# Optimization experiments

Measured on AMD Instinct MI355X. Metric: run time of the kernel, lower is better.

The kernel has to match this reference:

```python
import jax, jax.numpy as jnp
import numpy as np

BLOCK_SIZE = 128   # b
NUM_STEPS = 3      # T


def setup_inputs() -> dict:
    key = jax.random.key(0)
    kq, kk, kv = jax.random.split(key, 3)
    B, H, N, D = 4, 16, 8192, 64
    return {
        "query": jax.random.normal(kq, (B, H, N, D), jnp.float32),
        "key": jax.random.normal(kk, (B, H, N, D), jnp.float32),
        "value": jax.random.normal(kv, (B, H, N, D), jnp.float32),
    }


def reference(query, key, value):
    """Monarch attention: approximate softmax attention with a Monarch-factorized
    matrix M[(i,l),(k,l')] = L_l[i,k] * R_k[l,l'] (L: b blocks of m x m, R: m blocks
    of b x b, both row-stochastic), refined by NUM_STEPS alternating softmax updates.
    Never materializes the N x N attention matrix.
    """
    b, T = BLOCK_SIZE, NUM_STEPS
    B, H, N, D = query.shape
    m = N // b  # number of blocks; N assumed divisible by b (pad otherwise)
    scale = 1.0 / jnp.sqrt(jnp.asarray(D, query.dtype))
    eps = jnp.asarray(1e-6, query.dtype)

    Qb = query.reshape(B, H, m, b, D)   # token n = i*b + l -> (i, l)
    Kb = key.reshape(B, H, m, b, D)
    Vb = value.reshape(B, H, m, b, D)

    # init: uniform R  =>  Kbar[k,l] = mean_{l'} K[k,l'] (l-independent)
    Kbar = jnp.broadcast_to(Kb.mean(axis=3, keepdims=True), Qb.shape)  # (B,H,m,b,D)

    L = R = None
    for _ in range(T):
        # --- L update: L_l[i,k] = softmax_k( <Q[i,l], Kbar[k,l]> / sqrt(D) ) ---
        scores_L = scale * jnp.einsum('bhild,bhkld->bhlik', Qb, Kbar)  # (B,H,b,m,m)
        L = jax.nn.softmax(scores_L, axis=-1)
        # --- R update: weighted-average query per (k,l), then softmax over keys in block k ---
        w = jnp.sum(L, axis=-2)                                        # (B,H,b,m) = sum_i L_l[i,k]
        Qbar = jnp.einsum('bhlik,bhild->bhkld', L, Qb) / (jnp.swapaxes(w, -1, -2)[..., None] + eps)
        scores_R = scale * jnp.einsum('bhkld,bhked->bhkle', Qbar, Kb)  # (B,H,m,b,b) [k,l,l']
        R = jax.nn.softmax(scores_R, axis=-1)
        # refresh block-summarized keys for next L update
        Kbar = jnp.einsum('bhkle,bhked->bhkld', R, Kb)                 # (B,H,m,b,D)

    # output: out[(i,l)] = sum_k L_l[i,k] * (sum_{l'} R_k[l,l'] V[k,l'])
    Vbar = jnp.einsum('bhkle,bhked->bhkld', R, Vb)                     # (B,H,m,b,D)
    out = jnp.einsum('bhlik,bhkld->bhild', L, Vbar)                    # (B,H,m,b,D)
    return out.reshape(B, H, N, D)
```

## Files before the change

kernel.cpp:

```cpp
#include <hip/hip_runtime.h>
#include <stdint.h>


#define BH   64
#define NTOK 8192
#define DD   64
#define MM   64
#define BBS  128

typedef __attribute__((ext_vector_type(8))) short bf16x8;
typedef __attribute__((ext_vector_type(4))) float f32x4;

union U8 { bf16x8 v; uint32_t u[4]; };

__device__ __forceinline__ f32x4 MF(bf16x8 a, bf16x8 b, f32x4 c){
    return __builtin_amdgcn_mfma_f32_16x16x32_bf16(a, b, c, 0, 0, 0);
}
__device__ __forceinline__ f32x4 MF3(bf16x8 ah, bf16x8 al, bf16x8 bh_, bf16x8 bl_, f32x4 c){
    c = MF(ah, bh_, c);
    c = MF(ah, bl_, c);
    c = MF(al, bh_, c);
    return c;
}

__device__ __forceinline__ ushort bf16h(float x){
    union{float f; uint32_t u;} v; v.f = x;
    return (ushort)((v.u + 0x7fffu + ((v.u >> 16) & 1u)) >> 16);
}
__device__ __forceinline__ float bf16f(ushort h){
    union{float f; uint32_t u;} v; v.u = ((uint32_t)h) << 16; return v.f;
}
__device__ __forceinline__ void split2(float x, ushort& h, ushort& l){
    h = bf16h(x);
    l = bf16h(x - bf16f(h));
}
__device__ __forceinline__ uint32_t packsplit(float x){
    ushort h, l; split2(x, h, l);
    return ((uint32_t)h << 16) | (uint32_t)l;
}
__device__ __forceinline__ void st2(ushort* p, ushort a, ushort b){
    *(uint32_t*)p = (uint32_t)a | ((uint32_t)b << 16);
}
__device__ __forceinline__ void pack2(float a, float b, uint32_t& hw, uint32_t& lw){
    ushort ah_, al_, bh2, bl2;
    split2(a, ah_, al_); split2(b, bh2, bl2);
    hw = (uint32_t)ah_ | ((uint32_t)bh2 << 16);
    lw = (uint32_t)al_ | ((uint32_t)bl2 << 16);
}

__device__ __forceinline__ float red16_max(float v){
    v = fmaxf(v, __shfl_xor(v, 1));
    v = fmaxf(v, __shfl_xor(v, 2));
    v = fmaxf(v, __shfl_xor(v, 4));
    v = fmaxf(v, __shfl_xor(v, 8));
    return v;
}
__device__ __forceinline__ float red16_sum(float v){
    v += __shfl_xor(v, 1);
    v += __shfl_xor(v, 2);
    v += __shfl_xor(v, 4);
    v += __shfl_xor(v, 8);
    return v;
}

__device__ __forceinline__ void tr4x4(int qpos, float x0, float x1, float x2, float x3,
                                      float& z0, float& z1, float& z2, float& z3){
    float s1 = (qpos&1) ? x0 : x1; float g1 = __shfl_xor(s1, 16);
    float s2 = (qpos&1) ? x2 : x3; float g2 = __shfl_xor(s2, 16);
    float y0 = (qpos&1) ? g1 : x0;
    float y1 = (qpos&1) ? x1 : g1;
    float y2 = (qpos&1) ? g2 : x2;
    float y3 = (qpos&1) ? x3 : g2;
    float u1 = (qpos&2) ? y0 : y2; float h1 = __shfl_xor(u1, 32);
    float u2 = (qpos&2) ? y1 : y3; float h2 = __shfl_xor(u2, 32);
    z0 = (qpos&2) ? h1 : y0;
    z2 = (qpos&2) ? y2 : h1;
    z1 = (qpos&2) ? h2 : y1;
    z3 = (qpos&2) ? y3 : h2;
}

__global__ __launch_bounds__(256) void kbar0_kernel(const float* __restrict__ K,
                                                    float* __restrict__ kbar0){
    const int k = blockIdx.x, bh = blockIdx.y;
    const int t = threadIdx.x;
    const int d = t & 63, p = t >> 6;
    __shared__ float part[4][64];
    const float* base = K + ((size_t)bh*NTOK + (size_t)k*BBS)*DD + d;
    float s = 0.f;
    for(int lp = p*32; lp < p*32 + 32; ++lp) s += base[(size_t)lp*DD];
    part[p][d] = s;
    __syncthreads();
    if(t < 64){
        float tot = part[0][t] + part[1][t] + part[2][t] + part[3][t];
        kbar0[((size_t)bh*MM + k)*DD + t] = tot * (1.0f/128.0f);
    }
}

__global__ __launch_bounds__(256, 4) void l_kernel(const float* __restrict__ Q,
                                                   const void* __restrict__ kb_in,
                                                   int mode, uint32_t* __restrict__ qbar){
    const int l = blockIdx.x, bh = blockIdx.y;
    const int t = threadIdx.x;
    __shared__ __align__(16) ushort sQTh[64*72], sQTl[64*72];
    __shared__ __align__(16) ushort sKh [64*72], sKl [64*72];
    __shared__ float wsum[64];
    ushort* sLTh = sKh; ushort* sLTl = sKl;

    if(t < 64) wsum[t] = 0.f;

    const int w4 = t >> 4;
    const int qpos = w4 & 3;
    const int dq = (t & 15) << 2;
    #pragma unroll
    for(int j=0;j<4;++j){
        int i  = j*16 + w4;
        int ib = j*16 + (w4 & ~3);
        float4 v = *(const float4*)(Q + ((size_t)bh*NTOK + (size_t)i*BBS + l)*DD + dq);
        float z0,z1,z2,z3;
        tr4x4(qpos, v.x, v.y, v.z, v.w, z0, z1, z2, z3);
        ushort h0,l0,h1,l1,h2,l2,h3,l3;
        split2(z0,h0,l0); split2(z1,h1,l1); split2(z2,h2,l2); split2(z3,h3,l3);
        int rowd = dq + qpos;
        st2(&sQTh[rowd*72 + ib],   h0,h1); st2(&sQTh[rowd*72 + ib+2], h2,h3);
        st2(&sQTl[rowd*72 + ib],   l0,l1); st2(&sQTl[rowd*72 + ib+2], l2,l3);
    }
    if(mode){
        const uint32_t* kp = (const uint32_t*)kb_in + ((size_t)bh*BBS + l)*(size_t)(MM*DD);
        #pragma unroll
        for(int j=0;j<8;++j){
            int f = (j*256+t)*2, k = f>>6, d = f&63;
            uint2 u = *(const uint2*)(kp + (size_t)k*DD + d);
            *(uint32_t*)&sKh[k*72+d] = (u.x >> 16)      | (u.y & 0xffff0000u);
            *(uint32_t*)&sKl[k*72+d] = (u.x & 0xffffu)  | (u.y << 16);
        }
    } else {
        const float* kp = (const float*)kb_in + (size_t)bh*(size_t)(MM*DD);
        #pragma unroll
        for(int j=0;j<4;++j){
            int idx = j*256+t, k = idx>>4, d = (idx&15)<<2;
            float4 v = *(const float4*)(kp + (size_t)k*DD + d);
            ushort h0,l0,h1,l1,h2,l2,h3,l3;
            split2(v.x,h0,l0); split2(v.y,h1,l1); split2(v.z,h2,l2); split2(v.w,h3,l3);
            st2(&sKh[k*72+d],   h0,h1); st2(&sKh[k*72+d+2], h2,h3);
            st2(&sKl[k*72+d],   l0,l1); st2(&sKl[k*72+d+2], l2,l3);
        }
    }
    __syncthreads();

    const int lane = t & 63, wv = t >> 6;
    const int n = lane & 15, qd = lane >> 4;
    const int m0 = wv * 16;

    f32x4 accS[4] = {};
    #pragma unroll
    for(int kb=0;kb<2;++kb){
        int co = kb*32 + qd*8;
        U8 ah, al;
        #pragma unroll
        for(int jj=0;jj<4;++jj){
            uint32_t a0 = sQTh[(co+2*jj  )*72 + m0+n];
            uint32_t a1 = sQTh[(co+2*jj+1)*72 + m0+n];
            ah.u[jj] = a0 | (a1<<16);
            uint32_t b0 = sQTl[(co+2*jj  )*72 + m0+n];
            uint32_t b1 = sQTl[(co+2*jj+1)*72 + m0+n];
            al.u[jj] = b0 | (b1<<16);
        }
        #pragma unroll
        for(int c=0;c<4;++c){
            bf16x8 bh_ = *(const bf16x8*)&sKh[(c*16+n)*72 + co];
            bf16x8 bl_ = *(const bf16x8*)&sKl[(c*16+n)*72 + co];
            accS[c] = MF3(ah.v, al.v, bh_, bl_, accS[c]);
        }
    }
    __syncthreads();

    float colp[4] = {0.f,0.f,0.f,0.f};
    #pragma unroll
    for(int r=0;r<4;++r){
        float vals[4]; float mx = -3.4e38f;
        #pragma unroll
        for(int c=0;c<4;++c){ vals[c] = accS[c][r]*0.125f; mx = fmaxf(mx, vals[c]); }
        mx = red16_max(mx);
        float s = 0.f;
        #pragma unroll
        for(int c=0;c<4;++c){ vals[c] = __expf(vals[c]-mx); s += vals[c]; }
        s = red16_sum(s);
        float inv = 1.0f/s;
        int irow = m0 + qd*4 + r;
        #pragma unroll
        for(int c=0;c<4;++c){
            float Lv = vals[c]*inv;
            colp[c] += Lv;
            ushort hh, ll; split2(Lv, hh, ll);
            sLTh[(c*16+n)*72 + irow] = hh;
            sLTl[(c*16+n)*72 + irow] = ll;
        }
    }
    #pragma unroll
    for(int c=0;c<4;++c){
        float v = colp[c];
        v += __shfl_xor(v,16); v += __shfl_xor(v,32);
        if(qd == 0) atomicAdd(&wsum[c*16+n], v);
    }
    __syncthreads();

    f32x4 accQ[4] = {};
    #pragma unroll
    for(int kb=0;kb<2;++kb){
        int co = kb*32 + qd*8;
        bf16x8 ah = *(const bf16x8*)&sLTh[(m0+n)*72 + co];
        bf16x8 al = *(const bf16x8*)&sLTl[(m0+n)*72 + co];
        #pragma unroll
        for(int dt2=0;dt2<4;++dt2){
            bf16x8 bh_ = *(const bf16x8*)&sQTh[(dt2*16+n)*72 + co];
            bf16x8 bl_ = *(const bf16x8*)&sQTl[(dt2*16+n)*72 + co];
            accQ[dt2] = MF3(ah, al, bh_, bl_, accQ[dt2]);
        }
    }
    uint32_t* qb = qbar + ((size_t)bh*BBS + l)*(size_t)(MM*DD);
    #pragma unroll
    for(int r=0;r<4;++r){
        int krow = m0 + qd*4 + r;
        float invw = 1.0f/(wsum[krow] + 1e-6f);
        #pragma unroll
        for(int dt2=0;dt2<4;++dt2){
            qb[(size_t)krow*DD + dt2*16 + n] = packsplit(accQ[dt2][r]*invw);
        }
    }
}

__global__ __launch_bounds__(512, 4) void r_kernel(const uint32_t* __restrict__ qbar,
                                                   const float* __restrict__ K,
                                                   const float* __restrict__ V,
                                                   uint32_t* __restrict__ outp, int outTok){
    const int k = blockIdx.x, bh = blockIdx.y;
    const int t = threadIdx.x;
    __shared__ __align__(16) ushort sm[32768];
    ushort* X1h = sm;
    ushort* X1l = sm + 8192;
    ushort* XTh = sm + 16384;
    ushort* XTl = sm + 24576;

    const int lane = t & 63, wv = t >> 6;
    const int n = lane & 15, qd = lane >> 4;
    const int m0 = wv * 16;

    const uint32_t* qrow = qbar + (size_t)bh*BBS*(size_t)(MM*DD) + (size_t)k*DD
                         + (size_t)(m0+n)*(size_t)(MM*DD);
    uint4 qa0 = *(const uint4*)(qrow + qd*8);
    uint4 qa1 = *(const uint4*)(qrow + qd*8 + 4);
    uint4 qa2 = *(const uint4*)(qrow + 32 + qd*8);
    uint4 qa3 = *(const uint4*)(qrow + 32 + qd*8 + 4);

    const float* kp = K + ((size_t)bh*NTOK + (size_t)k*BBS)*DD;
    const float* vp = V ? (V + ((size_t)bh*NTOK + (size_t)k*BBS)*DD) : kp;
    const int w4 = t >> 4;
    const int qpos = w4 & 3;
    const int dq = (t & 15) << 2;
    #pragma unroll
    for(int j=0;j<4;++j){
        int lp = j*32 + w4;
        float4 v = *(const float4*)(kp + (size_t)lp*DD + dq);
        ushort h0,l0,h1,l1,h2,l2,h3,l3;
        split2(v.x,h0,l0); split2(v.y,h1,l1); split2(v.z,h2,l2); split2(v.w,h3,l3);
        int e = ((lp>>2)<<8) + (((dq>>4)&3)<<6) + ((lp&3)<<4) + ((dq&15) ^ (((dq>>4)&1)<<3));
        st2(&X1h[e], h0,h1); st2(&X1h[e+2], h2,h3);
        st2(&X1l[e], l0,l1); st2(&X1l[e+2], l2,l3);

        float4 tv = v;
        if(V) tv = *(const float4*)(vp + (size_t)lp*DD + dq);
        float z0,z1,z2,z3;
        tr4x4(qpos, tv.x, tv.y, tv.z, tv.w, z0, z1, z2, z3);
        int dv = dq + qpos;
        int lb = j*32 + (w4 & ~3);
        ushort th0,tl0,th1,tl1,th2,tl2,th3,tl3;
        split2(z0,th0,tl0); split2(z1,th1,tl1); split2(z2,th2,tl2); split2(z3,th3,tl3);
        int eT = ((dv>>2)<<9) + ((lb>>4)<<6) + ((dv&3)<<4) + ((lb&15) ^ (((dv>>2)&1)<<3));
        st2(&XTh[eT], th0,th1); st2(&XTh[eT+2], th2,th3);
        st2(&XTl[eT], tl0,tl1); st2(&XTl[eT+2], tl2,tl3);
    }
    __syncthreads();

    U8 ah0, al0, ah1, al1;
    ah0.u[0] = (qa0.x>>16) | (qa0.y & 0xffff0000u);
    al0.u[0] = (qa0.x & 0xffffu) | (qa0.y<<16);
    ah0.u[1] = (qa0.z>>16) | (qa0.w & 0xffff0000u);
    al0.u[1] = (qa0.z & 0xffffu) | (qa0.w<<16);
    ah0.u[2] = (qa1.x>>16) | (qa1.y & 0xffff0000u);
    al0.u[2] = (qa1.x & 0xffffu) | (qa1.y<<16);
    ah0.u[3] = (qa1.z>>16) | (qa1.w & 0xffff0000u);
    al0.u[3] = (qa1.z & 0xffffu) | (qa1.w<<16);
    ah1.u[0] = (qa2.x>>16) | (qa2.y & 0xffff0000u);
    al1.u[0] = (qa2.x & 0xffffu) | (qa2.y<<16);
    ah1.u[1] = (qa2.z>>16) | (qa2.w & 0xffff0000u);
    al1.u[1] = (qa2.z & 0xffffu) | (qa2.w<<16);
    ah1.u[2] = (qa3.x>>16) | (qa3.y & 0xffff0000u);
    al1.u[2] = (qa3.x & 0xffffu) | (qa3.y<<16);
    ah1.u[3] = (qa3.z>>16) | (qa3.w & 0xffff0000u);
    al1.u[3] = (qa3.z & 0xffffu) | (qa3.w<<16);

    const int base1 = (n>>2)*256 + (n&3)*16 + ((qd>>1)<<6) + ((8*(qd&1)) ^ (8*((qd>>1)&1)));
    f32x4 accS[8] = {};
    #pragma unroll
    for(int c=0;c<8;++c){
        bf16x8 bh_ = *(const bf16x8*)&X1h[base1 + c*1024];
        bf16x8 bl_ = *(const bf16x8*)&X1l[base1 + c*1024];
        accS[c] = MF3(ah0.v, al0.v, bh_, bl_, accS[c]);
    }
    #pragma unroll
    for(int c=0;c<8;++c){
        bf16x8 bh_ = *(const bf16x8*)&X1h[base1 + c*1024 + 128];
        bf16x8 bl_ = *(const bf16x8*)&X1l[base1 + c*1024 + 128];
        accS[c] = MF3(ah1.v, al1.v, bh_, bl_, accS[c]);
    }

    #pragma unroll
    for(int r=0;r<4;++r){
        float vals[8]; float mx = -3.4e38f;
        #pragma unroll
        for(int c=0;c<8;++c){ vals[c] = accS[c][r]*0.125f; mx = fmaxf(mx, vals[c]); }
        mx = red16_max(mx);
        float s = 0.f;
        #pragma unroll
        for(int c=0;c<8;++c){ vals[c] = __expf(vals[c]-mx); s += vals[c]; }
        s = red16_sum(s);
        float inv = 1.0f/s;
        #pragma unroll
        for(int c=0;c<8;++c) accS[c][r] = vals[c]*inv;
    }
    __syncthreads();

    ushort* SWh = sm + wv*1280;
    ushort* SWl = SWh + 640;
    const int sw_rd = n*40 + qd*8;
    const int baseT = (n>>2)*512 + ((qd>>1)<<6) + (n&3)*16 + ((8*(qd&1)) ^ (8*((n>>2)&1)));
    f32x4 accO[4] = {};
    #pragma unroll
    for(int kb=0;kb<4;++kb){
        #pragma unroll
        for(int r=0;r<4;++r){
            #pragma unroll
            for(int c2=0;c2<2;++c2){
                ushort hh, ll;
                split2(accS[2*kb+c2][r], hh, ll);
                SWh[(qd*4+r)*40 + c2*16 + n] = hh;
                SWl[(qd*4+r)*40 + c2*16 + n] = ll;
            }
        }
        asm volatile("s_waitcnt lgkmcnt(0)" ::: "memory");
        __builtin_amdgcn_sched_barrier(0);
        bf16x8 ah2 = *(const bf16x8*)&SWh[sw_rd];
        bf16x8 al2 = *(const bf16x8*)&SWl[sw_rd];
        #pragma unroll
        for(int dt2=0;dt2<4;++dt2){
            bf16x8 bh_ = *(const bf16x8*)&XTh[baseT + dt2*2048 + kb*128];
            bf16x8 bl_ = *(const bf16x8*)&XTl[baseT + dt2*2048 + kb*128];
            accO[dt2] = MF3(ah2, al2, bh_, bl_, accO[dt2]);
        }
        asm volatile("" ::: "memory");
    }
    #pragma unroll
    for(int r=0;r<4;++r){
        int lrow = m0 + qd*4 + r;
        #pragma unroll
        for(int dt2=0;dt2<4;++dt2){
            uint32_t pw = packsplit(accO[dt2][r]);
            size_t off = outTok
                ? ((size_t)bh*NTOK + (size_t)k*BBS + lrow)*DD + dt2*16 + n
                : (((size_t)bh*BBS + lrow)*(size_t)MM + k)*DD + dt2*16 + n;
            outp[off] = pw;
        }
    }
}

__global__ __launch_bounds__(256, 4) void out_kernel(const float* __restrict__ Q,
                                                     const uint32_t* __restrict__ kbar,
                                                     float* __restrict__ out){
    const int l = blockIdx.x, bh = blockIdx.y;
    const int t = threadIdx.x;
    __shared__ __align__(16) ushort sKh [64*72], sKl [64*72];
    __shared__ __align__(16) ushort sVTh[64*72], sVTl[64*72];
    ushort* sLh = sKh; ushort* sLl = sKl;

    const int lane = t & 63, wv = t >> 6;
    const int n = lane & 15, qd = lane >> 4;
    const int m0 = wv * 16;

    const float* qr = Q + ((size_t)bh*NTOK + (size_t)(m0+n)*BBS + l)*DD;
    float4 qv0 = *(const float4*)(qr + qd*8);
    float4 qv1 = *(const float4*)(qr + qd*8 + 4);
    float4 qv2 = *(const float4*)(qr + 32 + qd*8);
    float4 qv3 = *(const float4*)(qr + 32 + qd*8 + 4);

    const uint32_t* kp = kbar + ((size_t)bh*BBS + l)*(size_t)(MM*DD);
    #pragma unroll
    for(int j=0;j<8;++j){
        int f = (j*256+t)*2, k = f>>6, d = f&63;
        uint2 u = *(const uint2*)(kp + (size_t)k*DD + d);
        *(uint32_t*)&sKh[k*72+d] = (u.x >> 16)     | (u.y & 0xffff0000u);
        *(uint32_t*)&sKl[k*72+d] = (u.x & 0xffffu) | (u.y << 16);
    }
    const uint32_t* vb = (const uint32_t*)out;
    #pragma unroll
    for(int j=0;j<16;++j){
        int idx = j*256+t, kk = idx>>6, d = idx&63;
        uint32_t u = vb[((size_t)bh*NTOK + (size_t)kk*BBS + l)*DD + d];
        sVTh[d*72+kk] = (ushort)(u >> 16);
        sVTl[d*72+kk] = (ushort)(u & 0xffffu);
    }
    __syncthreads();

    U8 ah0, al0, ah1, al1;
    pack2(qv0.x, qv0.y, ah0.u[0], al0.u[0]);
    pack2(qv0.z, qv0.w, ah0.u[1], al0.u[1]);
    pack2(qv1.x, qv1.y, ah0.u[2], al0.u[2]);
    pack2(qv1.z, qv1.w, ah0.u[3], al0.u[3]);
    pack2(qv2.x, qv2.y, ah1.u[0], al1.u[0]);
    pack2(qv2.z, qv2.w, ah1.u[1], al1.u[1]);
    pack2(qv3.x, qv3.y, ah1.u[2], al1.u[2]);
    pack2(qv3.z, qv3.w, ah1.u[3], al1.u[3]);

    f32x4 accS[4] = {};
    #pragma unroll
    for(int kb=0;kb<2;++kb){
        int co = kb*32 + qd*8;
        const bf16x8 ah = kb ? ah1.v : ah0.v;
        const bf16x8 al = kb ? al1.v : al0.v;
        #pragma unroll
        for(int c=0;c<4;++c){
            bf16x8 bh_ = *(const bf16x8*)&sKh[(c*16+n)*72 + co];
            bf16x8 bl_ = *(const bf16x8*)&sKl[(c*16+n)*72 + co];
            accS[c] = MF3(ah, al, bh_, bl_, accS[c]);
        }
    }
    __syncthreads();

    #pragma unroll
    for(int r=0;r<4;++r){
        float vals[4]; float mx = -3.4e38f;
        #pragma unroll
        for(int c=0;c<4;++c){ vals[c] = accS[c][r]*0.125f; mx = fmaxf(mx, vals[c]); }
        mx = red16_max(mx);
        float s = 0.f;
        #pragma unroll
        for(int c=0;c<4;++c){ vals[c] = __expf(vals[c]-mx); s += vals[c]; }
        s = red16_sum(s);
        float inv = 1.0f/s;
        int irow = m0 + qd*4 + r;
        #pragma unroll
        for(int c=0;c<4;++c){
            ushort hh, ll; split2(vals[c]*inv, hh, ll);
            sLh[irow*72 + c*16+n] = hh;
            sLl[irow*72 + c*16+n] = ll;
        }
    }
    __syncthreads();

    f32x4 accO[4] = {};
    #pragma unroll
    for(int kb=0;kb<2;++kb){
        int co = kb*32 + qd*8;
        bf16x8 ah = *(const bf16x8*)&sLh[(m0+n)*72 + co];
        bf16x8 al = *(const bf16x8*)&sLl[(m0+n)*72 + co];
        #pragma unroll
        for(int dt2=0;dt2<4;++dt2){
            bf16x8 bh_ = *(const bf16x8*)&sVTh[(dt2*16+n)*72 + co];
            bf16x8 bl_ = *(const bf16x8*)&sVTl[(dt2*16+n)*72 + co];
            accO[dt2] = MF3(ah, al, bh_, bl_, accO[dt2]);
        }
    }
    #pragma unroll
    for(int r=0;r<4;++r){
        int irow = m0 + qd*4 + r;
        #pragma unroll
        for(int dt2=0;dt2<4;++dt2){
            out[((size_t)bh*NTOK + (size_t)irow*BBS + l)*DD + dt2*16 + n] = accO[dt2][r];
        }
    }
}

extern "C" void kernel_launch(void* const* d_in, const int* in_sizes, int n_in,
                              void* d_out, int out_size, void* d_ws, size_t ws_size,
                              hipStream_t stream){
    const float* Q = (const float*)d_in[0];
    const float* K = (const float*)d_in[1];
    const float* V = (const float*)d_in[2];
    float* out = (float*)d_out;
    const size_t big = (size_t)BH * BBS * MM * DD;
    uint32_t* qbar  = (uint32_t*)d_ws;
    uint32_t* kbar  = qbar + big;
    float*    kbar0 = (float*)(kbar + big);

    kbar0_kernel<<<dim3(MM, BH), 256, 0, stream>>>(K, kbar0);
    l_kernel<<<dim3(BBS, BH), 256, 0, stream>>>(Q, kbar0, 0, qbar);
    r_kernel<<<dim3(MM, BH), 512, 0, stream>>>(qbar, K, nullptr, kbar, 0);
    l_kernel<<<dim3(BBS, BH), 256, 0, stream>>>(Q, kbar, 1, qbar);
    r_kernel<<<dim3(MM, BH), 512, 0, stream>>>(qbar, K, nullptr, kbar, 0);
    l_kernel<<<dim3(BBS, BH), 256, 0, stream>>>(Q, kbar, 1, qbar);
    r_kernel<<<dim3(MM, BH), 512, 0, stream>>>(qbar, K, V, (uint32_t*)out, 1);
    out_kernel<<<dim3(BBS, BH), 256, 0, stream>>>(Q, kbar, out);
}
```

Before: 1.022 ms.

## Cache pre-split bf16 Q/K in workspace, load Kbar fragments directly, swizzle LDS

```diff
diff --git a/kernel.cpp b/kernel.cpp
--- a/kernel.cpp
+++ b/kernel.cpp
@@ -41,11 +41,24 @@
 __device__ __forceinline__ void st2(ushort* p, ushort a, ushort b){
     *(uint32_t*)p = (uint32_t)a | ((uint32_t)b << 16);
 }
+__device__ __forceinline__ void up2(uint32_t w0, uint32_t w1, uint32_t& hw, uint32_t& lw){
+    hw = (w0 >> 16)     | (w1 & 0xffff0000u);
+    lw = (w0 & 0xffffu) | (w1 << 16);
+}
 __device__ __forceinline__ void pack2(float a, float b, uint32_t& hw, uint32_t& lw){
     ushort ah_, al_, bh2, bl2;
     split2(a, ah_, al_); split2(b, bh2, bl2);
     hw = (uint32_t)ah_ | ((uint32_t)bh2 << 16);
     lw = (uint32_t)al_ | ((uint32_t)bl2 << 16);
+}
+__device__ __forceinline__ int swz8(int row){
+    return ((((row & 3) << 1) ^ ((row >> 2) & 7)) << 3);
+}
+__device__ __forceinline__ void frag_pk(uint4 a, uint4 b, bf16x8& h, bf16x8& l){
+    U8 H, L;
+    up2(a.x,a.y,H.u[0],L.u[0]); up2(a.z,a.w,H.u[1],L.u[1]);
+    up2(b.x,b.y,H.u[2],L.u[2]); up2(b.z,b.w,H.u[3],L.u[3]);
+    h = H.v; l = L.v;
 }
 
 __device__ __forceinline__ float red16_max(float v){
@@ -63,16 +76,16 @@
     return v;
 }
 
-__device__ __forceinline__ void tr4x4(int qpos, float x0, float x1, float x2, float x3,
-                                      float& z0, float& z1, float& z2, float& z3){
-    float s1 = (qpos&1) ? x0 : x1; float g1 = __shfl_xor(s1, 16);
-    float s2 = (qpos&1) ? x2 : x3; float g2 = __shfl_xor(s2, 16);
-    float y0 = (qpos&1) ? g1 : x0;
-    float y1 = (qpos&1) ? x1 : g1;
-    float y2 = (qpos&1) ? g2 : x2;
-    float y3 = (qpos&1) ? x3 : g2;
-    float u1 = (qpos&2) ? y0 : y2; float h1 = __shfl_xor(u1, 32);
-    float u2 = (qpos&2) ? y1 : y3; float h2 = __shfl_xor(u2, 32);
+__device__ __forceinline__ void tr4x4u(int qpos, uint32_t x0, uint32_t x1, uint32_t x2, uint32_t x3,
+                                       uint32_t& z0, uint32_t& z1, uint32_t& z2, uint32_t& z3){
+    uint32_t s1 = (qpos&1) ? x0 : x1; uint32_t g1 = (uint32_t)__shfl_xor((int)s1, 16);
+    uint32_t s2 = (qpos&1) ? x2 : x3; uint32_t g2 = (uint32_t)__shfl_xor((int)s2, 16);
+    uint32_t y0 = (qpos&1) ? g1 : x0;
+    uint32_t y1 = (qpos&1) ? x1 : g1;
+    uint32_t y2 = (qpos&1) ? g2 : x2;
+    uint32_t y3 = (qpos&1) ? x3 : g2;
+    uint32_t u1 = (qpos&2) ? y0 : y2; uint32_t h1 = (uint32_t)__shfl_xor((int)u1, 32);
+    uint32_t u2 = (qpos&2) ? y1 : y3; uint32_t h2 = (uint32_t)__shfl_xor((int)u2, 32);
     z0 = (qpos&2) ? h1 : y0;
     z2 = (qpos&2) ? y2 : h1;
     z1 = (qpos&2) ? h2 : y1;
@@ -80,99 +93,113 @@
 }
 
 __global__ __launch_bounds__(256) void kbar0_kernel(const float* __restrict__ K,
-                                                    float* __restrict__ kbar0){
+                                                    uint32_t* __restrict__ kbar0p,
+                                                    uint32_t* __restrict__ kpk){
     const int k = blockIdx.x, bh = blockIdx.y;
     const int t = threadIdx.x;
     const int d = t & 63, p = t >> 6;
     __shared__ float part[4][64];
     const float* base = K + ((size_t)bh*NTOK + (size_t)k*BBS)*DD + d;
+    uint32_t* kpb = kpk ? kpk + ((size_t)bh*NTOK + (size_t)k*BBS)*DD + d : nullptr;
     float s = 0.f;
-    for(int lp = p*32; lp < p*32 + 32; ++lp) s += base[(size_t)lp*DD];
+    for(int lp = p*32; lp < p*32 + 32; ++lp){
+        float v = base[(size_t)lp*DD];
+        s += v;
+        if(kpb) kpb[(size_t)lp*DD] = packsplit(v);
+    }
     part[p][d] = s;
     __syncthreads();
     if(t < 64){
         float tot = part[0][t] + part[1][t] + part[2][t] + part[3][t];
-        kbar0[((size_t)bh*MM + k)*DD + t] = tot * (1.0f/128.0f);
+        kbar0p[((size_t)bh*MM + k)*DD + t] = packsplit(tot * (1.0f/128.0f));
     }
 }
 
 __global__ __launch_bounds__(256, 4) void l_kernel(const float* __restrict__ Q,
-                                                   const void* __restrict__ kb_in,
-                                                   int mode, uint32_t* __restrict__ qbar){
+                                                   const uint32_t* __restrict__ kb_in,
+                                                   int mode,
+                                                   const uint32_t* __restrict__ qpk_ld,
+                                                   uint32_t* __restrict__ qpk_st,
+                                                   uint32_t* __restrict__ qbar){
     const int l = blockIdx.x, bh = blockIdx.y;
     const int t = threadIdx.x;
-    __shared__ __align__(16) ushort sQTh[64*72], sQTl[64*72];
-    __shared__ __align__(16) ushort sKh [64*72], sKl [64*72];
+    __shared__ __align__(16) ushort sQTh[4096], sQTl[4096];
+    __shared__ __align__(16) ushort sLTh[4096], sLTl[4096];
     __shared__ float wsum[64];
-    ushort* sLTh = sKh; ushort* sLTl = sKl;
+
+    const int lane = t & 63, wv = t >> 6;
+    const int n = lane & 15, qd = lane >> 4;
+    const int m0 = wv * 16;
 
     if(t < 64) wsum[t] = 0.f;
 
-    const int w4 = t >> 4;
-    const int qpos = w4 & 3;
-    const int dq = (t & 15) << 2;
+    U8 ah0, al0, ah1, al1;
+    const size_t qoff = ((size_t)bh*NTOK + (size_t)(m0+n)*BBS + l)*DD;
+    if(qpk_ld){
+        uint4 a0 = *(const uint4*)(qpk_ld + qoff + qd*8);
+        uint4 a1 = *(const uint4*)(qpk_ld + qoff + qd*8 + 4);
+        uint4 a2 = *(const uint4*)(qpk_ld + qoff + 32 + qd*8);
+        uint4 a3 = *(const uint4*)(qpk_ld + qoff + 32 + qd*8 + 4);
+        up2(a0.x,a0.y,ah0.u[0],al0.u[0]); up2(a0.z,a0.w,ah0.u[1],al0.u[1]);
+        up2(a1.x,a1.y,ah0.u[2],al0.u[2]); up2(a1.z,a1.w,ah0.u[3],al0.u[3]);
+        up2(a2.x,a2.y,ah1.u[0],al1.u[0]); up2(a2.z,a2.w,ah1.u[1],al1.u[1]);
+        up2(a3.x,a3.y,ah1.u[2],al1.u[2]); up2(a3.z,a3.w,ah1.u[3],al1.u[3]);
+    } else {
+        float4 qv0 = *(const float4*)(Q + qoff + qd*8);
+        float4 qv1 = *(const float4*)(Q + qoff + qd*8 + 4);
+        float4 qv2 = *(const float4*)(Q + qoff + 32 + qd*8);
+        float4 qv3 = *(const float4*)(Q + qoff + 32 + qd*8 + 4);
+        pack2(qv0.x,qv0.y,ah0.u[0],al0.u[0]); pack2(qv0.z,qv0.w,ah0.u[1],al0.u[1]);
+        pack2(qv1.x,qv1.y,ah0.u[2],al0.u[2]); pack2(qv1.z,qv1.w,ah0.u[3],al0.u[3]);
+        pack2(qv2.x,qv2.y,ah1.u[0],al1.u[0]); pack2(qv2.z,qv2.w,ah1.u[1],al1.u[1]);
+        pack2(qv3.x,qv3.y,ah1.u[2],al1.u[2]); pack2(qv3.z,qv3.w,ah1.u[3],al1.u[3]);
+    }
+
+    const int w4 = t >> 4, qpos = w4 & 3, dq = (t & 15) << 2;
     #pragma unroll
     for(int j=0;j<4;++j){
         int i  = j*16 + w4;
         int ib = j*16 + (w4 & ~3);
-        float4 v = *(const float4*)(Q + ((size_t)bh*NTOK + (size_t)i*BBS + l)*DD + dq);
-        float z0,z1,z2,z3;
-        tr4x4(qpos, v.x, v.y, v.z, v.w, z0, z1, z2, z3);
-        ushort h0,l0,h1,l1,h2,l2,h3,l3;
-        split2(z0,h0,l0); split2(z1,h1,l1); split2(z2,h2,l2); split2(z3,h3,l3);
+        size_t off = ((size_t)bh*NTOK + (size_t)i*BBS + l)*DD + dq;
+        uint32_t p0,p1,p2,p3v;
+        if(qpk_ld){
+            uint4 u = *(const uint4*)(qpk_ld + off);
+            p0=u.x; p1=u.y; p2=u.z; p3v=u.w;
+        } else {
+            float4 v = *(const float4*)(Q + off);
+            p0=packsplit(v.x); p1=packsplit(v.y); p2=packsplit(v.z); p3v=packsplit(v.w);
+            if(qpk_st){
+                uint4 uu; uu.x=p0; uu.y=p1; uu.z=p2; uu.w=p3v;
+                *(uint4*)(qpk_st + off) = uu;
+            }
+        }
+        uint32_t z0,z1,z2,z3;
+        tr4x4u(qpos, p0,p1,p2,p3v, z0,z1,z2,z3);
         int rowd = dq + qpos;
-        st2(&sQTh[rowd*72 + ib],   h0,h1); st2(&sQTh[rowd*72 + ib+2], h2,h3);
-        st2(&sQTl[rowd*72 + ib],   l0,l1); st2(&sQTl[rowd*72 + ib+2], l2,l3);
-    }
-    if(mode){
-        const uint32_t* kp = (const uint32_t*)kb_in + ((size_t)bh*BBS + l)*(size_t)(MM*DD);
-        #pragma unroll
-        for(int j=0;j<8;++j){
-            int f = (j*256+t)*2, k = f>>6, d = f&63;
-            uint2 u = *(const uint2*)(kp + (size_t)k*DD + d);
-            *(uint32_t*)&sKh[k*72+d] = (u.x >> 16)      | (u.y & 0xffff0000u);
-            *(uint32_t*)&sKl[k*72+d] = (u.x & 0xffffu)  | (u.y << 16);
-        }
-    } else {
-        const float* kp = (const float*)kb_in + (size_t)bh*(size_t)(MM*DD);
-        #pragma unroll
-        for(int j=0;j<4;++j){
-            int idx = j*256+t, k = idx>>4, d = (idx&15)<<2;
-            float4 v = *(const float4*)(kp + (size_t)k*DD + d);
-            ushort h0,l0,h1,l1,h2,l2,h3,l3;
-            split2(v.x,h0,l0); split2(v.y,h1,l1); split2(v.z,h2,l2); split2(v.w,h3,l3);
-            st2(&sKh[k*72+d],   h0,h1); st2(&sKh[k*72+d+2], h2,h3);
-            st2(&sKl[k*72+d],   l0,l1); st2(&sKl[k*72+d+2], l2,l3);
-        }
-    }
-    __syncthreads();
-
-    const int lane = t & 63, wv = t >> 6;
-    const int n = lane & 15, qd = lane >> 4;
-    const int m0 = wv * 16;
-
+        int e = rowd*64 + (ib ^ swz8(rowd));
+        st2(&sQTh[e],   (ushort)(z0>>16), (ushort)(z1>>16));
+        st2(&sQTh[e+2], (ushort)(z2>>16), (ushort)(z3>>16));
+        st2(&sQTl[e],   (ushort)(z0&0xffffu), (ushort)(z1&0xffffu));
+        st2(&sQTl[e+2], (ushort)(z2&0xffffu), (ushort)(z3&0xffffu));
+    }
+    __syncthreads();
+
+    const uint32_t* kb_base = mode ? kb_in + ((size_t)bh*BBS + l)*(size_t)(MM*DD)
+                                   : kb_in + (size_t)bh*(size_t)(MM*DD);
     f32x4 accS[4] = {};
     #pragma unroll
     for(int kb=0;kb<2;++kb){
-        int co = kb*32 + qd*8;
-        U8 ah, al;
-        #pragma unroll
-        for(int jj=0;jj<4;++jj){
-            uint32_t a0 = sQTh[(co+2*jj  )*72 + m0+n];
-            uint32_t a1 = sQTh[(co+2*jj+1)*72 + m0+n];
-            ah.u[jj] = a0 | (a1<<16);
-            uint32_t b0 = sQTl[(co+2*jj  )*72 + m0+n];
-            uint32_t b1 = sQTl[(co+2*jj+1)*72 + m0+n];
-            al.u[jj] = b0 | (b1<<16);
-        }
+        bf16x8 ah = kb ? ah1.v : ah0.v;
+        bf16x8 al = kb ? al1.v : al0.v;
         #pragma unroll
         for(int c=0;c<4;++c){
-            bf16x8 bh_ = *(const bf16x8*)&sKh[(c*16+n)*72 + co];
-            bf16x8 bl_ = *(const bf16x8*)&sKl[(c*16+n)*72 + co];
-            accS[c] = MF3(ah.v, al.v, bh_, bl_, accS[c]);
-        }
-    }
-    __syncthreads();
+            const uint32_t* fp = kb_base + (size_t)(c*16+n)*DD + kb*32 + qd*8;
+            uint4 b0 = *(const uint4*)fp;
+            uint4 b1 = *(const uint4*)(fp + 4);
+            bf16x8 bh_, bl_; frag_pk(b0, b1, bh_, bl_);
+            accS[c] = MF3(ah, al, bh_, bl_, accS[c]);
+        }
+    }
 
     float colp[4] = {0.f,0.f,0.f,0.f};
     #pragma unroll
@@ -192,8 +219,9 @@
             float Lv = vals[c]*inv;
             colp[c] += Lv;
             ushort hh, ll; split2(Lv, hh, ll);
-            sLTh[(c*16+n)*72 + irow] = hh;
-            sLTl[(c*16+n)*72 + irow] = ll;
+            int row = c*16+n;
+            sLTh[row*64 + (irow ^ swz8(row))] = hh;
+            sLTl[row*64 + (irow ^ swz8(row))] = ll;
         }
     }
     #pragma unroll
@@ -208,12 +236,14 @@
     #pragma unroll
     for(int kb=0;kb<2;++kb){
         int co = kb*32 + qd*8;
-        bf16x8 ah = *(const bf16x8*)&sLTh[(m0+n)*72 + co];
-        bf16x8 al = *(const bf16x8*)&sLTl[(m0+n)*72 + co];
+        int ra = m0 + n;
+        bf16x8 ah = *(const bf16x8*)&sLTh[ra*64 + (co ^ swz8(ra))];
+        bf16x8 al = *(const bf16x8*)&sLTl[ra*64 + (co ^ swz8(ra))];
         #pragma unroll
         for(int dt2=0;dt2<4;++dt2){
-            bf16x8 bh_ = *(const bf16x8*)&sQTh[(dt2*16+n)*72 + co];
-            bf16x8 bl_ = *(const bf16x8*)&sQTl[(dt2*16+n)*72 + co];
+            int rb = dt2*16 + n;
+            bf16x8 bh_ = *(const bf16x8*)&sQTh[rb*64 + (co ^ swz8(rb))];
+            bf16x8 bl_ = *(const bf16x8*)&sQTl[rb*64 + (co ^ swz8(rb))];
             accQ[dt2] = MF3(ah, al, bh_, bl_, accQ[dt2]);
         }
     }
@@ -229,88 +259,65 @@
     }
 }
 
-__global__ __launch_bounds__(512, 4) void r_kernel(const uint32_t* __restrict__ qbar,
+__global__ __launch_bounds__(512, 6) void r_kernel(const uint32_t* __restrict__ qbar,
                                                    const float* __restrict__ K,
+                                                   const uint32_t* __restrict__ kpk,
                                                    const float* __restrict__ V,
                                                    uint32_t* __restrict__ outp, int outTok){
     const int k = blockIdx.x, bh = blockIdx.y;
     const int t = threadIdx.x;
-    __shared__ __align__(16) ushort sm[32768];
+    __shared__ __align__(16) ushort sm[26624];
     ushort* X1h = sm;
     ushort* X1l = sm + 8192;
-    ushort* XTh = sm + 16384;
-    ushort* XTl = sm + 24576;
 
     const int lane = t & 63, wv = t >> 6;
     const int n = lane & 15, qd = lane >> 4;
     const int m0 = wv * 16;
 
-    const uint32_t* qrow = qbar + (size_t)bh*BBS*(size_t)(MM*DD) + (size_t)k*DD
-                         + (size_t)(m0+n)*(size_t)(MM*DD);
+    const uint32_t* qrow = qbar + (size_t)bh*BBS*(size_t)(MM*DD)
+                         + (size_t)(m0+n)*(size_t)(MM*DD) + (size_t)k*DD;
     uint4 qa0 = *(const uint4*)(qrow + qd*8);
     uint4 qa1 = *(const uint4*)(qrow + qd*8 + 4);
     uint4 qa2 = *(const uint4*)(qrow + 32 + qd*8);
     uint4 qa3 = *(const uint4*)(qrow + 32 + qd*8 + 4);
 
-    const float* kp = K + ((size_t)bh*NTOK + (size_t)k*BBS)*DD;
-    const float* vp = V ? (V + ((size_t)bh*NTOK + (size_t)k*BBS)*DD) : kp;
-    const int w4 = t >> 4;
-    const int qpos = w4 & 3;
-    const int dq = (t & 15) << 2;
+    const int w4 = t >> 4, qpos = w4 & 3, dq = (t & 15) << 2;
+    const size_t kboff = ((size_t)bh*NTOK + (size_t)k*BBS)*DD;
     #pragma unroll
     for(int j=0;j<4;++j){
         int lp = j*32 + w4;
-        float4 v = *(const float4*)(kp + (size_t)lp*DD + dq);
-        ushort h0,l0,h1,l1,h2,l2,h3,l3;
-        split2(v.x,h0,l0); split2(v.y,h1,l1); split2(v.z,h2,l2); split2(v.w,h3,l3);
-        int e = ((lp>>2)<<8) + (((dq>>4)&3)<<6) + ((lp&3)<<4) + ((dq&15) ^ (((dq>>4)&1)<<3));
-        st2(&X1h[e], h0,h1); st2(&X1h[e+2], h2,h3);
-        st2(&X1l[e], l0,l1); st2(&X1l[e+2], l2,l3);
-
-        float4 tv = v;
-        if(V) tv = *(const float4*)(vp + (size_t)lp*DD + dq);
-        float z0,z1,z2,z3;
-        tr4x4(qpos, tv.x, tv.y, tv.z, tv.w, z0, z1, z2, z3);
-        int dv = dq + qpos;
-        int lb = j*32 + (w4 & ~3);
-        ushort th0,tl0,th1,tl1,th2,tl2,th3,tl3;
-        split2(z0,th0,tl0); split2(z1,th1,tl1); split2(z2,th2,tl2); split2(z3,th3,tl3);
-        int eT = ((dv>>2)<<9) + ((lb>>4)<<6) + ((dv&3)<<4) + ((lb&15) ^ (((dv>>2)&1)<<3));
-        st2(&XTh[eT], th0,th1); st2(&XTh[eT+2], th2,th3);
-        st2(&XTl[eT], tl0,tl1); st2(&XTl[eT+2], tl2,tl3);
+        uint32_t p0,p1,p2,p3v;
+        if(kpk){
+            uint4 u = *(const uint4*)(kpk + kboff + (size_t)lp*DD + dq);
+            p0=u.x; p1=u.y; p2=u.z; p3v=u.w;
+        } else {
+            float4 v = *(const float4*)(K + kboff + (size_t)lp*DD + dq);
+            p0=packsplit(v.x); p1=packsplit(v.y); p2=packsplit(v.z); p3v=packsplit(v.w);
+        }
+        int e = lp*64 + (dq ^ swz8(lp));
+        *(uint32_t*)&X1h[e]   = (p0>>16)     | (p1 & 0xffff0000u);
+        *(uint32_t*)&X1h[e+2] = (p2>>16)     | (p3v & 0xffff0000u);
+        *(uint32_t*)&X1l[e]   = (p0&0xffffu) | (p1 << 16);
+        *(uint32_t*)&X1l[e+2] = (p2&0xffffu) | (p3v << 16);
     }
     __syncthreads();
 
     U8 ah0, al0, ah1, al1;
-    ah0.u[0] = (qa0.x>>16) | (qa0.y & 0xffff0000u);
-    al0.u[0] = (qa0.x & 0xffffu) | (qa0.y<<16);
-    ah0.u[1] = (qa0.z>>16) | (qa0.w & 0xffff0000u);
-    al0.u[1] = (qa0.z & 0xffffu) | (qa0.w<<16);
-    ah0.u[2] = (qa1.x>>16) | (qa1.y & 0xffff0000u);
-    al0.u[2] = (qa1.x & 0xffffu) | (qa1.y<<16);
-    ah0.u[3] = (qa1.z>>16) | (qa1.w & 0xffff0000u);
-    al0.u[3] = (qa1.z & 0xffffu) | (qa1.w<<16);
-    ah1.u[0] = (qa2.x>>16) | (qa2.y & 0xffff0000u);
-    al1.u[0] = (qa2.x & 0xffffu) | (qa2.y<<16);
-    ah1.u[1] = (qa2.z>>16) | (qa2.w & 0xffff0000u);
-    al1.u[1] = (qa2.z & 0xffffu) | (qa2.w<<16);
-    ah1.u[2] = (qa3.x>>16) | (qa3.y & 0xffff0000u);
-    al1.u[2] = (qa3.x & 0xffffu) | (qa3.y<<16);
-    ah1.u[3] = (qa3.z>>16) | (qa3.w & 0xffff0000u);
-    al1.u[3] = (qa3.z & 0xffffu) | (qa3.w<<16);
-
-    const int base1 = (n>>2)*256 + (n&3)*16 + ((qd>>1)<<6) + ((8*(qd&1)) ^ (8*((qd>>1)&1)));
+    up2(qa0.x,qa0.y,ah0.u[0],al0.u[0]); up2(qa0.z,qa0.w,ah0.u[1],al0.u[1]);
+    up2(qa1.x,qa1.y,ah0.u[2],al0.u[2]); up2(qa1.z,qa1.w,ah0.u[3],al0.u[3]);
+    up2(qa2.x,qa2.y,ah1.u[0],al1.u[0]); up2(qa2.z,qa2.w,ah1.u[1],al1.u[1]);
+    up2(qa3.x,qa3.y,ah1.u[2],al1.u[2]); up2(qa3.z,qa3.w,ah1.u[3],al1.u[3]);
+
     f32x4 accS[8] = {};
     #pragma unroll
     for(int c=0;c<8;++c){
-        bf16x8 bh_ = *(const bf16x8*)&X1h[base1 + c*1024];
-        bf16x8 bl_ = *(const bf16x8*)&X1l[base1 + c*1024];
+        int row = c*16 + n;
+        int bb = row*64, sw = swz8(row);
+        bf16x8 bh_ = *(const bf16x8*)&X1h[bb + ((qd*8) ^ sw)];
+        bf16x8 bl_ = *(const bf16x8*)&X1l[bb + ((qd*8) ^ sw)];
         accS[c] = MF3(ah0.v, al0.v, bh_, bl_, accS[c]);
-    }
-    #pragma unroll
-    for(int c=0;c<8;++c){
-        bf16x8 bh_ = *(const bf16x8*)&X1h[base1 + c*1024 + 128];
-        bf16x8 bl_ = *(const bf16x8*)&X1l[base1 + c*1024 + 128];
+        bh_ = *(const bf16x8*)&X1h[bb + ((32 + qd*8) ^ sw)];
+        bl_ = *(const bf16x8*)&X1l[bb + ((32 + qd*8) ^ sw)];
         accS[c] = MF3(ah1.v, al1.v, bh_, bl_, accS[c]);
     }
 
@@ -330,10 +337,37 @@
     }
     __syncthreads();
 
-    ushort* SWh = sm + wv*1280;
+    ushort* XTh = sm;
+    ushort* XTl = sm + 8192;
+    #pragma unroll
+    for(int j=0;j<4;++j){
+        int lp = j*32 + w4;
+        uint32_t p0,p1,p2,p3v;
+        if(V){
+            float4 v = *(const float4*)(V + kboff + (size_t)lp*DD + dq);
+            p0=packsplit(v.x); p1=packsplit(v.y); p2=packsplit(v.z); p3v=packsplit(v.w);
+        } else if(kpk){
+            uint4 u = *(const uint4*)(kpk + kboff + (size_t)lp*DD + dq);
+            p0=u.x; p1=u.y; p2=u.z; p3v=u.w;
+        } else {
+            float4 v = *(const float4*)(K + kboff + (size_t)lp*DD + dq);
+            p0=packsplit(v.x); p1=packsplit(v.y); p2=packsplit(v.z); p3v=packsplit(v.w);
+        }
+        uint32_t z0,z1,z2,z3;
+        tr4x4u(qpos, p0,p1,p2,p3v, z0,z1,z2,z3);
+        int dv = dq + qpos;
+        int lb = j*32 + (w4 & ~3);
+        int e = dv*128 + (lb ^ swz8(dv));
+        *(uint32_t*)&XTh[e]   = (z0>>16)     | (z1 & 0xffff0000u);
+        *(uint32_t*)&XTh[e+2] = (z2>>16)     | (z3 & 0xffff0000u);
+        *(uint32_t*)&XTl[e]   = (z0&0xffffu) | (z1 << 16);
+        *(uint32_t*)&XTl[e+2] = (z2&0xffffu) | (z3 << 16);
+    }
+    __syncthreads();
+
+    ushort* SWh = sm + 16384 + wv*1280;
     ushort* SWl = SWh + 640;
     const int sw_rd = n*40 + qd*8;
-    const int baseT = (n>>2)*512 + ((qd>>1)<<6) + (n&3)*16 + ((8*(qd&1)) ^ (8*((n>>2)&1)));
     f32x4 accO[4] = {};
     #pragma unroll
     for(int kb=0;kb<4;++kb){
@@ -353,8 +387,10 @@
         bf16x8 al2 = *(const bf16x8*)&SWl[sw_rd];
         #pragma unroll
         for(int dt2=0;dt2<4;++dt2){
-            bf16x8 bh_ = *(const bf16x8*)&XTh[baseT + dt2*2048 + kb*128];
-            bf16x8 bl_ = *(const bf16x8*)&XTl[baseT + dt2*2048 + kb*128];
+            int row = dt2*16 + n;
+            int e2 = row*128 + ((kb*32 + qd*8) ^ swz8(row));
+            bf16x8 bh_ = *(const bf16x8*)&XTh[e2];
+            bf16x8 bl_ = *(const bf16x8*)&XTl[e2];
             accO[dt2] = MF3(ah2, al2, bh_, bl_, accO[dt2]);
         }
         asm volatile("" ::: "memory");
@@ -374,66 +410,72 @@
 }
 
 __global__ __launch_bounds__(256, 4) void out_kernel(const float* __restrict__ Q,
+                                                     const uint32_t* __restrict__ qpk_ld,
                                                      const uint32_t* __restrict__ kbar,
                                                      float* __restrict__ out){
     const int l = blockIdx.x, bh = blockIdx.y;
     const int t = threadIdx.x;
-    __shared__ __align__(16) ushort sKh [64*72], sKl [64*72];
-    __shared__ __align__(16) ushort sVTh[64*72], sVTl[64*72];
-    ushort* sLh = sKh; ushort* sLl = sKl;
+    __shared__ __align__(16) ushort sVTh[4096], sVTl[4096];
+    __shared__ __align__(16) ushort swb[5120];
 
     const int lane = t & 63, wv = t >> 6;
     const int n = lane & 15, qd = lane >> 4;
     const int m0 = wv * 16;
 
-    const float* qr = Q + ((size_t)bh*NTOK + (size_t)(m0+n)*BBS + l)*DD;
-    float4 qv0 = *(const float4*)(qr + qd*8);
-    float4 qv1 = *(const float4*)(qr + qd*8 + 4);
-    float4 qv2 = *(const float4*)(qr + 32 + qd*8);
-    float4 qv3 = *(const float4*)(qr + 32 + qd*8 + 4);
-
-    const uint32_t* kp = kbar + ((size_t)bh*BBS + l)*(size_t)(MM*DD);
-    #pragma unroll
-    for(int j=0;j<8;++j){
-        int f = (j*256+t)*2, k = f>>6, d = f&63;
-        uint2 u = *(const uint2*)(kp + (size_t)k*DD + d);
-        *(uint32_t*)&sKh[k*72+d] = (u.x >> 16)     | (u.y & 0xffff0000u);
-        *(uint32_t*)&sKl[k*72+d] = (u.x & 0xffffu) | (u.y << 16);
-    }
+    U8 ah0, al0, ah1, al1;
+    const size_t qoff = ((size_t)bh*NTOK + (size_t)(m0+n)*BBS + l)*DD;
+    if(qpk_ld){
+        uint4 a0 = *(const uint4*)(qpk_ld + qoff + qd*8);
+        uint4 a1 = *(const uint4*)(qpk_ld + qoff + qd*8 + 4);
+        uint4 a2 = *(const uint4*)(qpk_ld + qoff + 32 + qd*8);
+        uint4 a3 = *(const uint4*)(qpk_ld + qoff + 32 + qd*8 + 4);
+        up2(a0.x,a0.y,ah0.u[0],al0.u[0]); up2(a0.z,a0.w,ah0.u[1],al0.u[1]);
+        up2(a1.x,a1.y,ah0.u[2],al0.u[2]); up2(a1.z,a1.w,ah0.u[3],al0.u[3]);
+        up2(a2.x,a2.y,ah1.u[0],al1.u[0]); up2(a2.z,a2.w,ah1.u[1],al1.u[1]);
+        up2(a3.x,a3.y,ah1.u[2],al1.u[2]); up2(a3.z,a3.w,ah1.u[3],al1.u[3]);
+    } else {
+        float4 qv0 = *(const float4*)(Q + qoff + qd*8);
+        float4 qv1 = *(const float4*)(Q + qoff + qd*8 + 4);
+        float4 qv2 = *(const float4*)(Q + qoff + 32 + qd*8);
+        float4 qv3 = *(const float4*)(Q + qoff + 32 + qd*8 + 4);
+        pack2(qv0.x,qv0.y,ah0.u[0],al0.u[0]); pack2(qv0.z,qv0.w,ah0.u[1],al0.u[1]);
+        pack2(qv1.x,qv1.y,ah0.u[2],al0.u[2]); pack2(qv1.z,qv1.w,ah0.u[3],al0.u[3]);
+        pack2(qv2.x,qv2.y,ah1.u[0],al1.u[0]); pack2(qv2.z,qv2.w,ah1.u[1],al1.u[1]);
+        pack2(qv3.x,qv3.y,ah1.u[2],al1.u[2]); pack2(qv3.z,qv3.w,ah1.u[3],al1.u[3]);
+    }
+
+    const int w4 = t >> 4, qpos = w4 & 3, dq = (t & 15) << 2;
     const uint32_t* vb = (const uint32_t*)out;
     #pragma unroll
-    for(int j=0;j<16;++j){
-        int idx = j*256+t, kk = idx>>6, d = idx&63;
-        uint32_t u = vb[((size_t)bh*NTOK + (size_t)kk*BBS + l)*DD + d];
-        sVTh[d*72+kk] = (ushort)(u >> 16);
-        sVTl[d*72+kk] = (ushort)(u & 0xffffu);
-    }
-    __syncthreads();
-
-    U8 ah0, al0, ah1, al1;
-    pack2(qv0.x, qv0.y, ah0.u[0], al0.u[0]);
-    pack2(qv0.z, qv0.w, ah0.u[1], al0.u[1]);
-    pack2(qv1.x, qv1.y, ah0.u[2], al0.u[2]);
-    pack2(qv1.z, qv1.w, ah0.u[3], al0.u[3]);
-    pack2(qv2.x, qv2.y, ah1.u[0], al1.u[0]);
-    pack2(qv2.z, qv2.w, ah1.u[1], al1.u[1]);
-    pack2(qv3.x, qv3.y, ah1.u[2], al1.u[2]);
-    pack2(qv3.z, qv3.w, ah1.u[3], al1.u[3]);
-
+    for(int j=0;j<4;++j){
+        int kk = j*16 + w4;
+        uint4 u = *(const uint4*)(vb + ((size_t)bh*NTOK + (size_t)kk*BBS + l)*DD + dq);
+        uint32_t z0,z1,z2,z3;
+        tr4x4u(qpos, u.x,u.y,u.z,u.w, z0,z1,z2,z3);
+        int dv = dq + qpos;
+        int kb4 = j*16 + (w4 & ~3);
+        int e = dv*64 + (kb4 ^ swz8(dv));
+        st2(&sVTh[e],   (ushort)(z0>>16), (ushort)(z1>>16));
+        st2(&sVTh[e+2], (ushort)(z2>>16), (ushort)(z3>>16));
+        st2(&sVTl[e],   (ushort)(z0&0xffffu), (ushort)(z1&0xffffu));
+        st2(&sVTl[e+2], (ushort)(z2&0xffffu), (ushort)(z3&0xffffu));
+    }
+
+    const uint32_t* kb_base = kbar + ((size_t)bh*BBS + l)*(size_t)(MM*DD);
     f32x4 accS[4] = {};
     #pragma unroll
     for(int kb=0;kb<2;++kb){
-        int co = kb*32 + qd*8;
-        const bf16x8 ah = kb ? ah1.v : ah0.v;
-        const bf16x8 al = kb ? al1.v : al0.v;
+        bf16x8 ah = kb ? ah1.v : ah0.v;
+        bf16x8 al = kb ? al1.v : al0.v;
         #pragma unroll
         for(int c=0;c<4;++c){
-            bf16x8 bh_ = *(const bf16x8*)&sKh[(c*16+n)*72 + co];
-            bf16x8 bl_ = *(const bf16x8*)&sKl[(c*16+n)*72 + co];
+            const uint32_t* fp = kb_base + (size_t)(c*16+n)*DD + kb*32 + qd*8;
+            uint4 b0 = *(const uint4*)fp;
+            uint4 b1 = *(const uint4*)(fp + 4);
+            bf16x8 bh_, bl_; frag_pk(b0, b1, bh_, bl_);
             accS[c] = MF3(ah, al, bh_, bl_, accS[c]);
         }
     }
-    __syncthreads();
 
     #pragma unroll
     for(int r=0;r<4;++r){
@@ -446,28 +488,40 @@
         for(int c=0;c<4;++c){ vals[c] = __expf(vals[c]-mx); s += vals[c]; }
         s = red16_sum(s);
         float inv = 1.0f/s;
-        int irow = m0 + qd*4 + r;
-        #pragma unroll
-        for(int c=0;c<4;++c){
-            ushort hh, ll; split2(vals[c]*inv, hh, ll);
-            sLh[irow*72 + c*16+n] = hh;
-            sLl[irow*72 + c*16+n] = ll;
-        }
-    }
-    __syncthreads();
-
+        #pragma unroll
+        for(int c=0;c<4;++c) accS[c][r] = vals[c]*inv;
+    }
+    __syncthreads();
+
+    ushort* SWh = swb + wv*1280;
+    ushort* SWl = SWh + 640;
+    const int sw_rd = n*40 + qd*8;
     f32x4 accO[4] = {};
     #pragma unroll
     for(int kb=0;kb<2;++kb){
-        int co = kb*32 + qd*8;
-        bf16x8 ah = *(const bf16x8*)&sLh[(m0+n)*72 + co];
-        bf16x8 al = *(const bf16x8*)&sLl[(m0+n)*72 + co];
+        #pragma unroll
+        for(int r=0;r<4;++r){
+            #pragma unroll
+            for(int c2=0;c2<2;++c2){
+                ushort hh, ll;
+                split2(accS[2*kb+c2][r], hh, ll);
+                SWh[(qd*4+r)*40 + c2*16 + n] = hh;
+                SWl[(qd*4+r)*40 + c2*16 + n] = ll;
+            }
+        }
+        asm volatile("s_waitcnt lgkmcnt(0)" ::: "memory");
+        __builtin_amdgcn_sched_barrier(0);
+        bf16x8 ah2 = *(const bf16x8*)&SWh[sw_rd];
+        bf16x8 al2 = *(const bf16x8*)&SWl[sw_rd];
         #pragma unroll
         for(int dt2=0;dt2<4;++dt2){
-            bf16x8 bh_ = *(const bf16x8*)&sVTh[(dt2*16+n)*72 + co];
-            bf16x8 bl_ = *(const bf16x8*)&sVTl[(dt2*16+n)*72 + co];
-            accO[dt2] = MF3(ah, al, bh_, bl_, accO[dt2]);
-        }
+            int row = dt2*16 + n;
+            int e2 = row*64 + ((kb*32 + qd*8) ^ swz8(row));
+            bf16x8 bh_ = *(const bf16x8*)&sVTh[e2];
+            bf16x8 bl_ = *(const bf16x8*)&sVTl[e2];
+            accO[dt2] = MF3(ah2, al2, bh_, bl_, accO[dt2]);
+        }
+        asm volatile("" ::: "memory");
     }
     #pragma unroll
     for(int r=0;r<4;++r){
@@ -487,16 +541,21 @@
     const float* V = (const float*)d_in[2];
     float* out = (float*)d_out;
     const size_t big = (size_t)BH * BBS * MM * DD;
-    uint32_t* qbar  = (uint32_t*)d_ws;
-    uint32_t* kbar  = qbar + big;
-    float*    kbar0 = (float*)(kbar + big);
-
-    kbar0_kernel<<<dim3(MM, BH), 256, 0, stream>>>(K, kbar0);
-    l_kernel<<<dim3(BBS, BH), 256, 0, stream>>>(Q, kbar0, 0, qbar);
-    r_kernel<<<dim3(MM, BH), 512, 0, stream>>>(qbar, K, nullptr, kbar, 0);
-    l_kernel<<<dim3(BBS, BH), 256, 0, stream>>>(Q, kbar, 1, qbar);
-    r_kernel<<<dim3(MM, BH), 512, 0, stream>>>(qbar, K, nullptr, kbar, 0);
-    l_kernel<<<dim3(BBS, BH), 256, 0, stream>>>(Q, kbar, 1, qbar);
-    r_kernel<<<dim3(MM, BH), 512, 0, stream>>>(qbar, K, V, (uint32_t*)out, 1);
-    out_kernel<<<dim3(BBS, BH), 256, 0, stream>>>(Q, kbar, out);
-}
+    const size_t kb0sz = (size_t)BH * MM * DD;
+    uint32_t* qbar   = (uint32_t*)d_ws;
+    uint32_t* kbar   = qbar + big;
+    uint32_t* kbar0p = kbar + big;
+    uint32_t* qpk    = kbar0p + kb0sz;
+    uint32_t* kpk    = qpk + big;
+    const size_t need_full = (2*big + kb0sz + 2*big) * 4ull;
+    if(ws_size < need_full){ qpk = nullptr; kpk = nullptr; }
+
+    kbar0_kernel<<<dim3(MM, BH), 256, 0, stream>>>(K, kbar0p, kpk);
+    l_kernel<<<dim3(BBS, BH), 256, 0, stream>>>(Q, kbar0p, 0, nullptr, qpk, qbar);
+    r_kernel<<<dim3(MM, BH), 512, 0, stream>>>(qbar, K, kpk, nullptr, kbar, 0);
+    l_kernel<<<dim3(BBS, BH), 256, 0, stream>>>(Q, kbar, 1, qpk, nullptr, qbar);
+    r_kernel<<<dim3(MM, BH), 512, 0, stream>>>(qbar, K, kpk, nullptr, kbar, 0);
+    l_kernel<<<dim3(BBS, BH), 256, 0, stream>>>(Q, kbar, 1, qpk, nullptr, qbar);
+    r_kernel<<<dim3(MM, BH), 512, 0, stream>>>(qbar, K, kpk, V, (uint32_t*)out, 1);
+    out_kernel<<<dim3(BBS, BH), 256, 0, stream>>>(Q, qpk, kbar, out);
+}
```

After: 1.277 ms. 1.25x slower.
